# Kernel tuning notes

Hardware: AMD Instinct MI355X
Metric: run time of the kernel (lower is better)

## Reference

```python
import jax, jax.numpy as jnp
import numpy as np

B = 128          # batch (requests)
SPEC = 4         # drafts per request (uniform here, code handles ragged)
V = 128000       # vocab size
MAX_SPEC_LEN = SPEC
NT = B * SPEC    # total flattened draft tokens
PLACEHOLDER = -1


def setup_inputs() -> dict:
    key = jax.random.key(0)
    k1, k2, k3, k4, k5 = jax.random.split(key, 5)
    draft_token_ids = jax.random.randint(k1, (NT,), 0, V, dtype=jnp.int32)
    draft_probs = jax.nn.softmax(2.0 * jax.random.normal(k2, (NT, V), dtype=jnp.float32), axis=-1)
    target_probs = jax.nn.softmax(2.0 * jax.random.normal(k3, (NT, V), dtype=jnp.float32), axis=-1)
    uniform_probs = jax.random.uniform(k4, (NT,), dtype=jnp.float32)
    bonus_token_ids = jax.random.randint(k5, (B,), 0, V, dtype=jnp.int32)
    cu_num_draft_tokens = (jnp.arange(1, B + 1) * SPEC).astype(jnp.int32)
    return {
        "draft_probs": draft_probs,
        "target_probs": target_probs,
        "uniform_probs": uniform_probs,
        "draft_token_ids": draft_token_ids,
        "cu_num_draft_tokens": cu_num_draft_tokens,
        "bonus_token_ids": bonus_token_ids,
    }


def reference(draft_probs, target_probs, uniform_probs, draft_token_ids,
              cu_num_draft_tokens, bonus_token_ids):
    # Faithful vectorized version of rejection_random_sample_kernel.
    nt = target_probs.shape[0]
    L = MAX_SPEC_LEN
    cu = cu_num_draft_tokens.astype(jnp.int32)
    prev = jnp.concatenate([jnp.zeros((1,), cu.dtype), cu[:-1]])   # start_idx per req
    ndraft = cu - prev                                              # [B]
    pos = jnp.arange(L, dtype=jnp.int32)                            # [L]
    tok_idx = prev[:, None] + pos[None, :]                          # [B,L] global token idx
    valid = pos[None, :] < ndraft[:, None]                          # [B,L]
    safe_idx = jnp.clip(tok_idx, 0, nt - 1)

    d_ids = draft_token_ids[safe_idx]                               # [B,L]
    tp = target_probs[safe_idx, d_ids]                              # target prob of draft token
    dp = draft_probs[safe_idx, d_ids]                               # draft prob of draft token
    uu = uniform_probs[safe_idx]

    # neutral values outside valid range: ratio=1, uniform=1 keep carries unchanged
    ratio = jnp.where(valid & (dp > 0), tp / jnp.where(dp > 0, dp, 1.0), 1.0)
    uu = jnp.where(valid, uu, 1.0)
    dpos = valid & (dp > 0)

    def step(carry, xs):
        pi, U = carry                       # [B] each
        r, u, ok = xs
        pi = jnp.minimum(pi * r, 1.0)
        U = U * u
        accept = ok & (pi >= U)
        return (pi, U), accept

    init = (jnp.ones((cu.shape[0],), jnp.float32), jnp.ones((cu.shape[0],), jnp.float32))
    _, accept = jax.lax.scan(step, init, (ratio.T, uu.T, dpos.T))   # accept: [L,B]
    accept = accept.T                                                # [B,L]

    # last accepted position (or -1); 'rejected' == final-iteration accept failed
    last = jnp.max(jnp.where(accept, pos[None, :], -1), axis=1)      # [B]
    rejected = (ndraft > 0) & (last != ndraft - 1)

    # copy accepted draft tokens [0..last]
    out_L = jnp.where(pos[None, :] <= last[:, None], d_ids, PLACEHOLDER).astype(jnp.int32)
    out = jnp.concatenate([out_L, jnp.full((cu.shape[0], 1), PLACEHOLDER, jnp.int32)], axis=1)

    # recovered token: argmax of target_probs row at position last+1
    rec_row = jnp.clip(prev + last + 1, 0, nt - 1)
    rec_id = jnp.argmax(target_probs[rec_row], axis=-1).astype(jnp.int32)   # [B]

    write_col = jnp.where(rejected, last + 1, ndraft)
    write_val = jnp.where(rejected, rec_id, bonus_token_ids.astype(jnp.int32))
    out = out.at[jnp.arange(cu.shape[0]), write_col].set(write_val)
    return out
```

## Files before the change

kernel.cpp:

```cpp
#include <hip/hip_runtime.h>
#include <hip/hip_bf16.h>
#include <float.h>

#define MAX_L 16

__global__ __launch_bounds__(256) void rejection_sample_kernel(
    const float* __restrict__ draft_probs,
    const float* __restrict__ target_probs,
    const float* __restrict__ uniform_probs,
    const int*   __restrict__ draft_ids,
    const int*   __restrict__ cu,
    const int*   __restrict__ bonus,
    int*         __restrict__ out,
    int B, int V, int NT, int L)
{
    const int b   = blockIdx.x;
    const int tid = threadIdx.x;

    __shared__ float s_tp[MAX_L], s_dp[MAX_L], s_u[MAX_L];
    __shared__ int   s_did[MAX_L];
    __shared__ int   s_rejected;
    __shared__ int   s_recrow;
    __shared__ int   s_writecol;

    const int start = (b == 0) ? 0 : cu[b - 1];
    const int nd    = cu[b] - start;
    const int nchain = (nd < L) ? nd : L;

    if (tid < nchain) {
        const int t   = start + tid;
        const int did = draft_ids[t];
        s_did[tid] = did;
        s_u[tid]   = uniform_probs[t];
        const size_t off = (size_t)t * (size_t)V + (size_t)did;
        s_tp[tid] = target_probs[off];
        s_dp[tid] = draft_probs[off];
    }
    __syncthreads();

    if (tid == 0) {
        float pi = 1.0f, U = 1.0f;
        int last = -1;
        for (int i = 0; i < nchain; ++i) {
            const float dpv = s_dp[i];
            const bool  ok  = dpv > 0.0f;
            const float r   = ok ? (s_tp[i] / dpv) : 1.0f;
            pi = fminf(pi * r, 1.0f);
            U  = U * s_u[i];
            if (ok && pi >= U) last = i;
        }
        const bool rejected = (nd > 0) && (last != nd - 1);
        int recrow = start + last + 1;
        recrow = recrow < 0 ? 0 : (recrow > NT - 1 ? NT - 1 : recrow);

        int* row = out + (size_t)b * (L + 1);
        for (int i = 0; i <= L; ++i) {
            row[i] = (i <= last) ? s_did[i] : -1;
        }
        if (!rejected) {
            row[nd] = bonus[b];
        }
        s_rejected = rejected ? 1 : 0;
        s_recrow   = recrow;
        s_writecol = last + 1;
    }
    __syncthreads();

    if (!s_rejected) return;

    const float4* rowp = (const float4*)(target_probs + (size_t)s_recrow * (size_t)V);
    const int n4 = V >> 2;
    float bestv = -FLT_MAX;
    int   besti = 0x7fffffff;
    for (int j = tid; j < n4; j += blockDim.x) {
        const float4 v = rowp[j];
        const int base = j << 2;
        if (v.x > bestv) { bestv = v.x; besti = base;     }
        if (v.y > bestv) { bestv = v.y; besti = base + 1; }
        if (v.z > bestv) { bestv = v.z; besti = base + 2; }
        if (v.w > bestv) { bestv = v.w; besti = base + 3; }
    }
    for (int j = (n4 << 2) + tid; j < V; j += blockDim.x) {
        const float v = target_probs[(size_t)s_recrow * (size_t)V + j];
        if (v > bestv) { bestv = v; besti = j; }
    }

    __shared__ float sv[256];
    __shared__ int   si[256];
    sv[tid] = bestv;
    si[tid] = besti;
    __syncthreads();
    for (int s = blockDim.x >> 1; s > 0; s >>= 1) {
        if (tid < s) {
            const float ov = sv[tid + s];
            const int   oi = si[tid + s];
            if (ov > sv[tid] || (ov == sv[tid] && oi < si[tid])) {
                sv[tid] = ov;
                si[tid] = oi;
            }
        }
        __syncthreads();
    }
    if (tid == 0) {
        out[(size_t)b * (L + 1) + s_writecol] = si[0];
    }
}

extern "C" void kernel_launch(void* const* d_in, const int* in_sizes, int n_in,
                              void* d_out, int out_size, void* d_ws, size_t ws_size,
                              hipStream_t stream) {
    const float* draft_probs   = (const float*)d_in[0];
    const float* target_probs  = (const float*)d_in[1];
    const float* uniform_probs = (const float*)d_in[2];
    const int*   draft_ids     = (const int*)d_in[3];
    const int*   cu            = (const int*)d_in[4];
    const int*   bonus         = (const int*)d_in[5];
    int*         out           = (int*)d_out;

    const int NT = in_sizes[2];
    const int V  = in_sizes[0] / NT;
    const int B  = in_sizes[4];
    const int L  = out_size / B - 1;

    rejection_sample_kernel<<<B, 256, 0, stream>>>(
        draft_probs, target_probs, uniform_probs, draft_ids, cu, bonus,
        out, B, V, NT, L);
}
```

Measured before the change: 451.0 us.

## Split argmax across multiple blocks per request with packed atomicMax reduction

The single-kernel design is replaced by three kernels. A per-request chain kernel runs one thread per request and writes the flags, the recovered row and the write column to workspace. An argmax kernel with a (B, 16) grid scans one slice of the row in each block and merges results through a 64-bit atomicMax on packed (value bits, inverted index). A finalize kernel writes the recovered token. This raises memory parallelism for the 128000-wide row scan, since the old kernel had only B=128 blocks. The cost is two extra kernel launches and a reliance on positive float bit ordering.

```diff
diff --git a/kernel.cpp b/kernel.cpp
--- a/kernel.cpp
+++ b/kernel.cpp
@@ -2,9 +2,10 @@
 #include <hip/hip_bf16.h>
 #include <float.h>
 
-#define MAX_L 16
+#define SPLITS 16
 
-__global__ __launch_bounds__(256) void rejection_sample_kernel(
+
+__global__ void chain_kernel(
     const float* __restrict__ draft_probs,
     const float* __restrict__ target_probs,
     const float* __restrict__ uniform_probs,
@@ -12,67 +13,72 @@
     const int*   __restrict__ cu,
     const int*   __restrict__ bonus,
     int*         __restrict__ out,
+    unsigned long long* __restrict__ packed,
+    int* __restrict__ flag, int* __restrict__ recrow, int* __restrict__ writecol,
     int B, int V, int NT, int L)
 {
-    const int b   = blockIdx.x;
-    const int tid = threadIdx.x;
-
-    __shared__ float s_tp[MAX_L], s_dp[MAX_L], s_u[MAX_L];
-    __shared__ int   s_did[MAX_L];
-    __shared__ int   s_rejected;
-    __shared__ int   s_recrow;
-    __shared__ int   s_writecol;
+    const int b = blockIdx.x * blockDim.x + threadIdx.x;
+    if (b >= B) return;
 
     const int start = (b == 0) ? 0 : cu[b - 1];
     const int nd    = cu[b] - start;
     const int nchain = (nd < L) ? nd : L;
 
-    if (tid < nchain) {
-        const int t   = start + tid;
+    float pi = 1.0f, U = 1.0f;
+    int last = -1;
+    int* row = out + (size_t)b * (L + 1);
+
+    for (int i = 0; i < nchain; ++i) {
+        const int t   = start + i;
         const int did = draft_ids[t];
-        s_did[tid] = did;
-        s_u[tid]   = uniform_probs[t];
+        row[i] = did;
         const size_t off = (size_t)t * (size_t)V + (size_t)did;
-        s_tp[tid] = target_probs[off];
-        s_dp[tid] = draft_probs[off];
+        const float tp = target_probs[off];
+        const float dp = draft_probs[off];
+        const float uu = uniform_probs[t];
+        const bool ok = dp > 0.0f;
+        const float r = ok ? (tp / dp) : 1.0f;
+        pi = fminf(pi * r, 1.0f);
+        U  = U * uu;
+        if (ok && pi >= U) last = i;
     }
-    __syncthreads();
+    for (int i = last + 1; i <= L; ++i) row[i] = -1;
 
-    if (tid == 0) {
-        float pi = 1.0f, U = 1.0f;
-        int last = -1;
-        for (int i = 0; i < nchain; ++i) {
-            const float dpv = s_dp[i];
-            const bool  ok  = dpv > 0.0f;
-            const float r   = ok ? (s_tp[i] / dpv) : 1.0f;
-            pi = fminf(pi * r, 1.0f);
-            U  = U * s_u[i];
-            if (ok && pi >= U) last = i;
-        }
-        const bool rejected = (nd > 0) && (last != nd - 1);
-        int recrow = start + last + 1;
-        recrow = recrow < 0 ? 0 : (recrow > NT - 1 ? NT - 1 : recrow);
+    const bool rejected = (nd > 0) && (last != nd - 1);
+    if (!rejected) {
+        row[nd] = bonus[b];
+    }
+    int rr = start + last + 1;
+    rr = rr < 0 ? 0 : (rr > NT - 1 ? NT - 1 : rr);
 
-        int* row = out + (size_t)b * (L + 1);
-        for (int i = 0; i <= L; ++i) {
-            row[i] = (i <= last) ? s_did[i] : -1;
-        }
-        if (!rejected) {
-            row[nd] = bonus[b];
-        }
-        s_rejected = rejected ? 1 : 0;
-        s_recrow   = recrow;
-        s_writecol = last + 1;
-    }
-    __syncthreads();
+    flag[b]     = rejected ? 1 : 0;
+    recrow[b]   = rr;
+    writecol[b] = last + 1;
+    packed[b]   = 0ull;
+}
 
-    if (!s_rejected) return;
+__global__ __launch_bounds__(256) void argmax_partial_kernel(
+    const float* __restrict__ target_probs,
+    const unsigned long long* __restrict__ ,
+    unsigned long long* __restrict__ packed,
+    const int* __restrict__ flag, const int* __restrict__ recrow,
+    int V)
+{
+    const int b = blockIdx.x;
+    const int s = blockIdx.y;
+    if (!flag[b]) return;
 
-    const float4* rowp = (const float4*)(target_probs + (size_t)s_recrow * (size_t)V);
+    const int tid = threadIdx.x;
+    const float* rowbase = target_probs + (size_t)recrow[b] * (size_t)V;
     const int n4 = V >> 2;
+    const int chunk4 = (n4 + SPLITS - 1) / SPLITS;
+    const int lo4 = s * chunk4;
+    const int hi4 = (lo4 + chunk4 < n4) ? lo4 + chunk4 : n4;
+
     float bestv = -FLT_MAX;
     int   besti = 0x7fffffff;
-    for (int j = tid; j < n4; j += blockDim.x) {
+    const float4* rowp = (const float4*)rowbase;
+    for (int j = lo4 + tid; j < hi4; j += 256) {
         const float4 v = rowp[j];
         const int base = j << 2;
         if (v.x > bestv) { bestv = v.x; besti = base;     }
@@ -80,9 +86,11 @@
         if (v.z > bestv) { bestv = v.z; besti = base + 2; }
         if (v.w > bestv) { bestv = v.w; besti = base + 3; }
     }
-    for (int j = (n4 << 2) + tid; j < V; j += blockDim.x) {
-        const float v = target_probs[(size_t)s_recrow * (size_t)V + j];
-        if (v > bestv) { bestv = v; besti = j; }
+    if (s == SPLITS - 1) {
+        for (int j = (n4 << 2) + tid; j < V; j += 256) {
+            const float v = rowbase[j];
+            if (v > bestv) { bestv = v; besti = j; }
+        }
     }
 
     __shared__ float sv[256];
@@ -90,10 +98,10 @@
     sv[tid] = bestv;
     si[tid] = besti;
     __syncthreads();
-    for (int s = blockDim.x >> 1; s > 0; s >>= 1) {
-        if (tid < s) {
-            const float ov = sv[tid + s];
-            const int   oi = si[tid + s];
+    for (int w = 128; w > 0; w >>= 1) {
+        if (tid < w) {
+            const float ov = sv[tid + w];
+            const int   oi = si[tid + w];
             if (ov > sv[tid] || (ov == sv[tid] && oi < si[tid])) {
                 sv[tid] = ov;
                 si[tid] = oi;
@@ -101,9 +109,27 @@
         }
         __syncthreads();
     }
-    if (tid == 0) {
-        out[(size_t)b * (L + 1) + s_writecol] = si[0];
+    if (tid == 0 && sv[0] > -FLT_MAX) {
+        const unsigned int fbits = __float_as_uint(sv[0]);
+        const unsigned long long p =
+            ((unsigned long long)fbits << 32) |
+            (unsigned long long)(0xFFFFFFFFu - (unsigned int)si[0]);
+        atomicMax(&packed[b], p);
     }
+}
+
+__global__ void finalize_kernel(
+    int* __restrict__ out,
+    const unsigned long long* __restrict__ packed,
+    const int* __restrict__ flag, const int* __restrict__ writecol,
+    int B, int L)
+{
+    const int b = blockIdx.x * blockDim.x + threadIdx.x;
+    if (b >= B) return;
+    if (!flag[b]) return;
+    const unsigned long long p = packed[b];
+    const int idx = (int)(0xFFFFFFFFu - (unsigned int)(p & 0xFFFFFFFFull));
+    out[(size_t)b * (L + 1) + writecol[b]] = idx;
 }
 
 extern "C" void kernel_launch(void* const* d_in, const int* in_sizes, int n_in,
@@ -122,7 +148,22 @@
     const int B  = in_sizes[4];
     const int L  = out_size / B - 1;
 
-    rejection_sample_kernel<<<B, 256, 0, stream>>>(
+    unsigned long long* packed = (unsigned long long*)d_ws;
+    int* flag     = (int*)((char*)d_ws + (size_t)B * 8);
+    int* recrow   = (int*)((char*)d_ws + (size_t)B * 8 + (size_t)B * 4);
+    int* writecol = (int*)((char*)d_ws + (size_t)B * 8 + (size_t)B * 8);
+
+    const int bthreads = 256;
+    const int bblocks  = (B + bthreads - 1) / bthreads;
+
+    chain_kernel<<<bblocks, bthreads, 0, stream>>>(
         draft_probs, target_probs, uniform_probs, draft_ids, cu, bonus,
-        out, B, V, NT, L);
+        out, packed, flag, recrow, writecol, B, V, NT, L);
+
+    dim3 grid(B, SPLITS);
+    argmax_partial_kernel<<<grid, 256, 0, stream>>>(
+        target_probs, nullptr, packed, flag, recrow, V);
+
+    finalize_kernel<<<bblocks, bthreads, 0, stream>>>(
+        out, packed, flag, writecol, B, L);
 }
```

After: 408.4 us. 9.4% less time.
